# Optimization experiments

Hardware: AMD Instinct MI355X
Metric: run time of the kernel (lower is better)

The kernel has to match this reference:

```python
import jax, jax.numpy as jnp
import numpy as np

NUM_CLASSES = 1000
SMOOTHING = 0.1
CONFIDENCE = 1.0 - SMOOTHING
BATCH = 16384


def _smooth_matrix():
    """Precompute [C, C] matrix M where row c is the smoothed label vector for true class c.
    M[c, c] = confidence; M[c, k] = smoothing * w_ck / sum_j!=c w_cj with w = 1/(|k-c|+1)."""
    idx = jnp.arange(NUM_CLASSES)
    dist = jnp.abs(idx[:, None] - idx[None, :]).astype(jnp.float32)  # [C, C]
    w = 1.0 / (dist + 1.0)
    w = jnp.where(dist == 0, 0.0, w)               # exclude true class from weights
    total = w.sum(axis=1, keepdims=True)           # per-row normalizer
    M = SMOOTHING * (w / total)
    M = jnp.where(dist == 0, CONFIDENCE, M)
    return M.astype(jnp.float32)


def setup_inputs() -> dict:
    key = jax.random.key(0)
    k1, k2 = jax.random.split(key)
    logits = jax.random.normal(k1, (BATCH, NUM_CLASSES), dtype=jnp.float32)
    targets = jax.random.randint(k2, (BATCH,), 0, NUM_CLASSES)
    return {"logits": logits, "targets": targets}


def reference(logits, targets):
    # logits: [B, C], targets: [B] int
    log_probs = jax.nn.log_softmax(logits, axis=1)        # [B, C]
    smooth_labels = _smooth_matrix()[targets]             # gather rows -> [B, C]
    loss = -(smooth_labels * log_probs).sum(axis=1).mean()
    return loss
```

## Files before the change

kernel.cpp:

```cpp
#include <hip/hip_runtime.h>
#include <math.h>

#define NUM_CLASSES 1000
#define NV4 250
#define BATCH 16384
#define NBLOCKS (BATCH / 4)

__global__ __launch_bounds__(256) void row_loss_kernel(
    const float* __restrict__ logits,
    const int* __restrict__ targets,
    float* __restrict__ partials) {
  const int wave = threadIdx.x >> 6;
  const int lane = threadIdx.x & 63;
  const int b = blockIdx.x * 4 + wave;

  const float4* row = (const float4*)(logits + (size_t)b * NUM_CLASSES);
  const int c = __builtin_amdgcn_readfirstlane(targets[b]);

  float4 v[4];
#pragma unroll
  for (int i = 0; i < 4; ++i) {
    const int j = lane + 64 * i;
    if (j < NV4) v[i] = row[j];
    else v[i] = make_float4(-INFINITY, -INFINITY, -INFINITY, -INFINITY);
  }

  float m = -INFINITY;
#pragma unroll
  for (int i = 0; i < 4; ++i)
    m = fmaxf(m, fmaxf(fmaxf(v[i].x, v[i].y), fmaxf(v[i].z, v[i].w)));

  float se = 0.f;
  float ws = 0.f;
  float tw = 0.f;
  float lc = 0.f;
#pragma unroll
  for (int i = 0; i < 4; ++i) {
    const float xs[4] = {v[i].x, v[i].y, v[i].z, v[i].w};
    const int k0 = (lane + 64 * i) * 4;
#pragma unroll
    for (int e = 0; e < 4; ++e) {
      const int k = k0 + e;
      const float x = xs[e];
      se += __expf(x - m);
      if (k < NUM_CLASSES) {
        if (k == c) {
          lc = x;
        } else {
          const float w = __builtin_amdgcn_rcpf((float)(abs(k - c) + 1));
          ws = fmaf(w, x, ws);
          tw += w;
        }
      }
    }
  }

#pragma unroll
  for (int o = 32; o > 0; o >>= 1) {
    const float mo  = __shfl_xor(m, o);
    const float seo = __shfl_xor(se, o);
    const float wso = __shfl_xor(ws, o);
    const float two = __shfl_xor(tw, o);
    const float lco = __shfl_xor(lc, o);
    const float nm = fmaxf(m, mo);
    se = se * __expf(m - nm) + seo * __expf(mo - nm);
    m = nm;
    ws += wso;
    tw += two;
    lc += lco;
  }

  __shared__ float sw[4];
  if (lane == 0) {
    sw[wave] = m + __logf(se) - (0.9f * lc + 0.1f * (ws / tw));
  }
  __syncthreads();
  if (threadIdx.x == 0) {
    partials[blockIdx.x] = (sw[0] + sw[1]) + (sw[2] + sw[3]);
  }
}

__global__ __launch_bounds__(256) void final_reduce_kernel(
    const float4* __restrict__ partials, float* __restrict__ out) {
  float s = 0.f;
#pragma unroll
  for (int i = 0; i < NBLOCKS / 4 / 256; ++i) {
    const float4 t = partials[threadIdx.x + 256 * i];
    s += (t.x + t.y) + (t.z + t.w);
  }
#pragma unroll
  for (int o = 32; o > 0; o >>= 1) s += __shfl_xor(s, o);
  __shared__ float sw[4];
  if ((threadIdx.x & 63) == 0) sw[threadIdx.x >> 6] = s;
  __syncthreads();
  if (threadIdx.x == 0) {
    out[0] = ((sw[0] + sw[1]) + (sw[2] + sw[3])) * (1.0f / (float)BATCH);
  }
}

extern "C" void kernel_launch(void* const* d_in, const int* in_sizes, int n_in,
                              void* d_out, int out_size, void* d_ws, size_t ws_size,
                              hipStream_t stream) {
  const float* logits = (const float*)d_in[0];
  const int* targets = (const int*)d_in[1];
  float* out = (float*)d_out;
  float* partials = (float*)d_ws;

  row_loss_kernel<<<NBLOCKS, 256, 0, stream>>>(logits, targets, partials);
  final_reduce_kernel<<<1, 256, 0, stream>>>((const float4*)partials, out);
}
```

Baseline: 92.49 us.

## Make per-element loss loop branchless and compute weight normalizer analytically

The inner loop drops its per-element branches on the true class and bounds. The weighted sum now includes the true class at weight 1 and subtracts it afterwards. The true-class logit is fetched with a single lane shuffle instead of being carried through the reduction. The weight normalizer is computed once per row from an asymptotic harmonic-number formula instead of being accumulated per element. Exponentials use exp2 with a fused multiply-add, and the sums are split into independent partial accumulators to shorten dependency chains. This cuts VALU work and shuffle traffic, at the cost of a small approximation error in the normalizer.

```diff
diff --git a/kernel.cpp b/kernel.cpp
--- a/kernel.cpp
+++ b/kernel.cpp
@@ -5,6 +5,13 @@
 #define NV4 250
 #define BATCH 16384
 #define NBLOCKS (BATCH / 4)
+#define LOG2E 1.44269504f
+
+#if __has_builtin(__builtin_amdgcn_exp2f)
+#define EXP2F(x) __builtin_amdgcn_exp2f(x)
+#else
+#define EXP2F(x) exp2f(x)
+#endif
 
 __global__ __launch_bounds__(256) void row_loss_kernel(
     const float* __restrict__ logits,
@@ -25,54 +32,66 @@
     else v[i] = make_float4(-INFINITY, -INFINITY, -INFINITY, -INFINITY);
   }
 
-  float m = -INFINITY;
-#pragma unroll
-  for (int i = 0; i < 4; ++i)
-    m = fmaxf(m, fmaxf(fmaxf(v[i].x, v[i].y), fmaxf(v[i].z, v[i].w)));
+  float ma = fmaxf(fmaxf(v[0].x, v[0].y), fmaxf(v[0].z, v[0].w));
+  float mb = fmaxf(fmaxf(v[1].x, v[1].y), fmaxf(v[1].z, v[1].w));
+  float mc_ = fmaxf(fmaxf(v[2].x, v[2].y), fmaxf(v[2].z, v[2].w));
+  float md = fmaxf(fmaxf(v[3].x, v[3].y), fmaxf(v[3].z, v[3].w));
+  float m = fmaxf(fmaxf(ma, mb), fmaxf(mc_, md));
 
-  float se = 0.f;
-  float ws = 0.f;
-  float tw = 0.f;
-  float lc = 0.f;
+  const float g = (float)(lane * 4) - (float)c;
+  const float hL = -m * LOG2E;
+
+  float se[4] = {0.f, 0.f, 0.f, 0.f};
+  float ws[4] = {0.f, 0.f, 0.f, 0.f};
 #pragma unroll
   for (int i = 0; i < 4; ++i) {
     const float xs[4] = {v[i].x, v[i].y, v[i].z, v[i].w};
-    const int k0 = (lane + 64 * i) * 4;
 #pragma unroll
     for (int e = 0; e < 4; ++e) {
-      const int k = k0 + e;
       const float x = xs[e];
-      se += __expf(x - m);
-      if (k < NUM_CLASSES) {
-        if (k == c) {
-          lc = x;
-        } else {
-          const float w = __builtin_amdgcn_rcpf((float)(abs(k - c) + 1));
-          ws = fmaf(w, x, ws);
-          tw += w;
-        }
-      }
+      se[i] += EXP2F(fmaf(x, LOG2E, hL));
+      const float t = g + (float)(256 * i + e);
+      const float w = __builtin_amdgcn_rcpf(fabsf(t) + 1.0f);
+      const float xw = (i == 3) ? ((lane < 58) ? x : 0.0f) : x;
+      ws[i] = fmaf(w, xw, ws[i]);
     }
   }
+  float seT = (se[0] + se[1]) + (se[2] + se[3]);
+  float wsT = (ws[0] + ws[1]) + (ws[2] + ws[3]);
+
+  const int ic = c >> 8;
+  const int ec = c & 3;
+  float4 vc;
+  if (ic == 0) vc = v[0];
+  else if (ic == 1) vc = v[1];
+  else if (ic == 2) vc = v[2];
+  else vc = v[3];
+  const float xl = (ec == 0) ? vc.x : (ec == 1) ? vc.y : (ec == 2) ? vc.z : vc.w;
+  const float lc = __shfl(xl, (c >> 2) & 63);
 
 #pragma unroll
   for (int o = 32; o > 0; o >>= 1) {
-    const float mo  = __shfl_xor(m, o);
-    const float seo = __shfl_xor(se, o);
-    const float wso = __shfl_xor(ws, o);
-    const float two = __shfl_xor(tw, o);
-    const float lco = __shfl_xor(lc, o);
+    const float mo = __shfl_xor(m, o);
+    const float so = __shfl_xor(seT, o);
+    const float wo = __shfl_xor(wsT, o);
     const float nm = fmaxf(m, mo);
-    se = se * __expf(m - nm) + seo * __expf(mo - nm);
+    seT = seT * EXP2F((m - nm) * LOG2E) + so * EXP2F((mo - nm) * LOG2E);
     m = nm;
-    ws += wso;
-    tw += two;
-    lc += lco;
+    wsT += wo;
   }
 
   __shared__ float sw[4];
   if (lane == 0) {
-    sw[wave] = m + __logf(se) - (0.9f * lc + 0.1f * (ws / tw));
+    const float n1 = (float)(c + 1);
+    const float n2 = (float)(NUM_CLASSES - c);
+    const float r1 = __builtin_amdgcn_rcpf(n1), r1s = r1 * r1;
+    const float r2 = __builtin_amdgcn_rcpf(n2), r2s = r2 * r2;
+    const float H1 = __logf(n1) + 0.57721566f + 0.5f * r1 -
+                     0.08333333f * r1s + 0.00833333f * r1s * r1s;
+    const float H2 = __logf(n2) + 0.57721566f + 0.5f * r2 -
+                     0.08333333f * r2s + 0.00833333f * r2s * r2s;
+    const float tw = H1 + H2 - 2.0f;
+    sw[wave] = m + __logf(seT) - (0.9f * lc + 0.1f * (wsT - lc) / tw);
   }
   __syncthreads();
   if (threadIdx.x == 0) {
```

Result: slower. 103.9 us (+12.3%).
